# Kernel optimization log

Hardware: AMD Instinct MI355X
Metric: run time of the kernel (lower is better)

## Reference

```python
import jax, jax.numpy as jnp
import numpy as np

N = 50000   # nodes
E = 600000  # edges
D = 128     # node_features (EvolveGCNO in=out channels)
H = 128     # hidden_dim (final Linear out)


def setup_inputs() -> dict:
    key = jax.random.key(0)
    ks = jax.random.split(key, 9)
    stdv = 1.0 / np.sqrt(D)
    u = lambda k, shape: jax.random.uniform(k, shape, jnp.float32, -stdv, stdv)
    return {
        "x": jax.random.normal(ks[0], (N, D), jnp.float32),
        "edge_index": jax.random.randint(ks[1], (2, E), 0, N),
        "edge_weight": jax.random.uniform(ks[2], (E,), jnp.float32),
        "W0": u(ks[3], (D, D)),        # EvolveGCNO initial_weight (squeezed)
        "w_ih": u(ks[4], (3 * D, D)),  # GRU input weights (r|z|n)
        "w_hh": u(ks[5], (3 * D, D)),  # GRU hidden weights (r|z|n)
        "b_ih": u(ks[6], (3 * D,)),
        "b_hh": u(ks[7], (3 * D,)),
        "W_lin": u(ks[8], (H, D)),     # torch Linear weight [out, in]
        "b_lin": jnp.zeros((H,), jnp.float32),
    }


def _gru_step(x, h, w_ih, w_hh, b_ih, b_hh):
    # One torch.nn.GRU cell step; here x == h == W0 (weight evolution).
    gi = x @ w_ih.T + b_ih
    gh = h @ w_hh.T + b_hh
    i_r, i_z, i_n = jnp.split(gi, 3, axis=-1)
    h_r, h_z, h_n = jnp.split(gh, 3, axis=-1)
    r = jax.nn.sigmoid(i_r + h_r)
    z = jax.nn.sigmoid(i_z + h_z)
    n = jnp.tanh(i_n + r * h_n)
    return (1.0 - z) * n + z * h


def reference(x, edge_index, edge_weight, W0, w_ih, w_hh, b_ih, b_hh, W_lin, b_lin):
    # 1) Evolve the GCN weight with one GRU step (input = hidden = W0).
    W = _gru_step(W0, W0, w_ih, w_hh, b_ih, b_hh)  # [D, D]

    # 2) GCNConv_Fixed_W: add self-loops (weight 1), symmetric normalization.
    loops = jnp.arange(N)
    row = jnp.concatenate([edge_index[0], loops])  # source
    col = jnp.concatenate([edge_index[1], loops])  # target
    ew = jnp.concatenate([edge_weight, jnp.ones((N,), x.dtype)])
    deg = jax.ops.segment_sum(ew, col, num_segments=N)
    dinv = jnp.where(deg > 0, jax.lax.rsqrt(deg), 0.0)
    norm = dinv[row] * ew * dinv[col]  # [E+N]

    xw = x @ W                                        # [N, D]
    h = jax.ops.segment_sum(norm[:, None] * xw[row], col, num_segments=N)  # [N, D]

    # 3) ReLU + Linear
    h = jax.nn.relu(h)
    return h @ W_lin.T + b_lin  # [N, H]
```

## Files before the change

### kernel.cpp

```cpp
#include <hip/hip_runtime.h>
#include <hip/hip_bf16.h>

#define NN 50000
#define EE 600000
#define DD 128
#define CAP 48
#define CNT_SHIFT 25
#define SUM_MASK 0x1FFFFFFu

typedef __attribute__((ext_vector_type(8))) __bf16 bf16x8;
typedef __attribute__((ext_vector_type(8))) short short8;
typedef __attribute__((ext_vector_type(4))) float f32x4;

__device__ __forceinline__ unsigned short f2bf(float f) {
    union { float f; unsigned u; } c; c.f = f;
    unsigned r = (c.u + 0x7fffu + ((c.u >> 16) & 1u)) >> 16;
    return (unsigned short)r;
}
__device__ __forceinline__ float bflo(unsigned u) {
    union { unsigned u; float f; } c; c.u = u << 16; return c.f;
}
__device__ __forceinline__ float bfhi(unsigned u) {
    union { unsigned u; float f; } c; c.u = u & 0xffff0000u; return c.f;
}
__device__ __forceinline__ float degof(unsigned p) {
    return 1.0f + (float)(p & SUM_MASK) * (1.0f / 65536.0f);
}

__global__ __launch_bounds__(256) void init_gru_kernel(
    unsigned* __restrict__ cnt32,
    const float* __restrict__ W0, const float* __restrict__ w_ih,
    const float* __restrict__ w_hh, const float* __restrict__ b_ih,
    const float* __restrict__ b_hh, unsigned short* __restrict__ Wbt)
{
    if (blockIdx.x < 49) {
        int i = blockIdx.x * 256 + threadIdx.x;
        if (i < 50176 * 4 / 16) ((uint4*)cnt32)[i] = make_uint4(0u, 0u, 0u, 0u);
        return;
    }
    int idx = (blockIdx.x - 49) * 256 + threadIdx.x;
    int i = idx >> 7, j = idx & 127;
    const float4* a  = (const float4*)(W0  + i * DD);
    const float4* pr = (const float4*)(w_ih + (j        ) * DD);
    const float4* pz = (const float4*)(w_ih + (j + 128  ) * DD);
    const float4* pn = (const float4*)(w_ih + (j + 256  ) * DD);
    const float4* qr = (const float4*)(w_hh + (j        ) * DD);
    const float4* qz = (const float4*)(w_hh + (j + 128  ) * DD);
    const float4* qn = (const float4*)(w_hh + (j + 256  ) * DD);
    float ir = 0.f, iz = 0.f, inn = 0.f, hr = 0.f, hz = 0.f, hn = 0.f;
    for (int d = 0; d < DD / 4; ++d) {
        float4 av = a[d];
        float4 t;
        t = pr[d]; ir  += av.x*t.x + av.y*t.y + av.z*t.z + av.w*t.w;
        t = pz[d]; iz  += av.x*t.x + av.y*t.y + av.z*t.z + av.w*t.w;
        t = pn[d]; inn += av.x*t.x + av.y*t.y + av.z*t.z + av.w*t.w;
        t = qr[d]; hr  += av.x*t.x + av.y*t.y + av.z*t.z + av.w*t.w;
        t = qz[d]; hz  += av.x*t.x + av.y*t.y + av.z*t.z + av.w*t.w;
        t = qn[d]; hn  += av.x*t.x + av.y*t.y + av.z*t.z + av.w*t.w;
    }
    ir += b_ih[j]; iz += b_ih[j + 128]; inn += b_ih[j + 256];
    hr += b_hh[j]; hz += b_hh[j + 128]; hn  += b_hh[j + 256];
    float r = 1.f / (1.f + expf(-(ir + hr)));
    float z = 1.f / (1.f + expf(-(iz + hz)));
    float n = tanhf(inn + r * hn);
    float w = (1.f - z) * n + z * W0[idx];
    Wbt[j * DD + i] = f2bf(w);
}

__global__ __launch_bounds__(256) void histfill_kernel(
    const int* __restrict__ row, const int* __restrict__ col,
    const float* __restrict__ ew,
    unsigned* __restrict__ cnt32, unsigned* __restrict__ edges)
{
    int e = blockIdx.x * 256 + threadIdx.x;
    if (e >= EE) return;
    int c = col[e];
    unsigned wq = (unsigned)(ew[e] * 65536.0f);
    if (wq > 65535u) wq = 65535u;
    unsigned old = atomicAdd(&cnt32[c], (1u << CNT_SHIFT) | wq);
    unsigned oldcnt = old >> CNT_SHIFT;
    if (oldcnt < CAP)
        edges[(size_t)c * CAP + oldcnt] = (unsigned)row[e] | (wq << 16);
}

__global__ __launch_bounds__(256) void gather_kernel(
    const unsigned* __restrict__ edges, const unsigned* __restrict__ cnt32,
    const unsigned* __restrict__ xwu, unsigned* __restrict__ hu)
{
    int wid  = threadIdx.x >> 6;
    int lane = threadIdx.x & 63;
    int node = blockIdx.x * 4 + wid;
    if (node >= NN) return;
    unsigned pn = cnt32[node];
    int n = (int)(pn >> CNT_SHIFT); if (n > CAP) n = CAP;
    const unsigned* eb = edges + (size_t)node * CAP;
    float ax = 0.f, ay = 0.f;
    int k = 0;
    int n8 = n & ~7;
    for (; k < n8; k += 8) {
        uint4 ra = *(const uint4*)(eb + k);
        uint4 rb = *(const uint4*)(eb + k + 4);
        int s0 = (int)(ra.x & 0xFFFFu), s1 = (int)(ra.y & 0xFFFFu);
        int s2 = (int)(ra.z & 0xFFFFu), s3 = (int)(ra.w & 0xFFFFu);
        int s4 = (int)(rb.x & 0xFFFFu), s5 = (int)(rb.y & 0xFFFFu);
        int s6 = (int)(rb.z & 0xFFFFu), s7 = (int)(rb.w & 0xFFFFu);
        unsigned p0 = cnt32[s0], p1 = cnt32[s1], p2 = cnt32[s2], p3 = cnt32[s3];
        unsigned p4 = cnt32[s4], p5 = cnt32[s5], p6 = cnt32[s6], p7 = cnt32[s7];
        unsigned x0 = xwu[(size_t)s0 * 64 + lane];
        unsigned x1 = xwu[(size_t)s1 * 64 + lane];
        unsigned x2 = xwu[(size_t)s2 * 64 + lane];
        unsigned x3 = xwu[(size_t)s3 * 64 + lane];
        unsigned x4 = xwu[(size_t)s4 * 64 + lane];
        unsigned x5 = xwu[(size_t)s5 * 64 + lane];
        unsigned x6 = xwu[(size_t)s6 * 64 + lane];
        unsigned x7 = xwu[(size_t)s7 * 64 + lane];
        float v0 = (float)(ra.x >> 16) * (1.0f / 65536.0f) * rsqrtf(degof(p0));
        float v1 = (float)(ra.y >> 16) * (1.0f / 65536.0f) * rsqrtf(degof(p1));
        float v2 = (float)(ra.z >> 16) * (1.0f / 65536.0f) * rsqrtf(degof(p2));
        float v3 = (float)(ra.w >> 16) * (1.0f / 65536.0f) * rsqrtf(degof(p3));
        float v4 = (float)(rb.x >> 16) * (1.0f / 65536.0f) * rsqrtf(degof(p4));
        float v5 = (float)(rb.y >> 16) * (1.0f / 65536.0f) * rsqrtf(degof(p5));
        float v6 = (float)(rb.z >> 16) * (1.0f / 65536.0f) * rsqrtf(degof(p6));
        float v7 = (float)(rb.w >> 16) * (1.0f / 65536.0f) * rsqrtf(degof(p7));
        ax += v0 * bflo(x0) + v1 * bflo(x1) + v2 * bflo(x2) + v3 * bflo(x3)
            + v4 * bflo(x4) + v5 * bflo(x5) + v6 * bflo(x6) + v7 * bflo(x7);
        ay += v0 * bfhi(x0) + v1 * bfhi(x1) + v2 * bfhi(x2) + v3 * bfhi(x3)
            + v4 * bfhi(x4) + v5 * bfhi(x5) + v6 * bfhi(x6) + v7 * bfhi(x7);
    }
    int n4 = n & ~3;
    for (; k < n4; k += 4) {
        uint4 rc = *(const uint4*)(eb + k);
        int s0 = (int)(rc.x & 0xFFFFu), s1 = (int)(rc.y & 0xFFFFu);
        int s2 = (int)(rc.z & 0xFFFFu), s3 = (int)(rc.w & 0xFFFFu);
        unsigned p0 = cnt32[s0], p1 = cnt32[s1], p2 = cnt32[s2], p3 = cnt32[s3];
        unsigned x0 = xwu[(size_t)s0 * 64 + lane];
        unsigned x1 = xwu[(size_t)s1 * 64 + lane];
        unsigned x2 = xwu[(size_t)s2 * 64 + lane];
        unsigned x3 = xwu[(size_t)s3 * 64 + lane];
        float v0 = (float)(rc.x >> 16) * (1.0f / 65536.0f) * rsqrtf(degof(p0));
        float v1 = (float)(rc.y >> 16) * (1.0f / 65536.0f) * rsqrtf(degof(p1));
        float v2 = (float)(rc.z >> 16) * (1.0f / 65536.0f) * rsqrtf(degof(p2));
        float v3 = (float)(rc.w >> 16) * (1.0f / 65536.0f) * rsqrtf(degof(p3));
        ax += v0 * bflo(x0) + v1 * bflo(x1) + v2 * bflo(x2) + v3 * bflo(x3);
        ay += v0 * bfhi(x0) + v1 * bfhi(x1) + v2 * bfhi(x2) + v3 * bfhi(x3);
    }
    for (; k < n; ++k) {
        unsigned r0 = eb[k];
        int s0 = (int)(r0 & 0xFFFFu);
        unsigned p0 = cnt32[s0];
        unsigned x0 = xwu[(size_t)s0 * 64 + lane];
        float v0 = (float)(r0 >> 16) * (1.0f / 65536.0f) * rsqrtf(degof(p0));
        ax += v0 * bflo(x0); ay += v0 * bfhi(x0);
    }
    float s = rsqrtf(degof(pn));
    hu[(size_t)node * 64 + lane] =
        (unsigned)f2bf(ax * s) | ((unsigned)f2bf(ay * s) << 16);
}

template <int MODE>
__global__ __launch_bounds__(256) void mfma_gemm(
    const float* __restrict__ Af, const short* __restrict__ hb,
    const short* __restrict__ xwb, const unsigned* __restrict__ cnt32,
    const short* __restrict__ Bb, const float* __restrict__ Bf,
    const float* __restrict__ bias,
    unsigned short* __restrict__ outb, float* __restrict__ outf)
{
    __shared__ __align__(16) short Bs[DD * DD];
    __shared__ __align__(16) short As[64 * DD];
    const int t = threadIdx.x;
    const int i0 = blockIdx.x * 64;

    if (MODE == 0) {
        for (int u = t; u < 2048; u += 256) {
            int byte = u << 4;
            int brow = byte >> 8;
            *(short8*)((char*)Bs + (byte ^ ((brow & 7) << 4))) =
                *(const short8*)((const char*)Bb + byte);
        }
    } else {
        for (int u = t; u < 2048; u += 256) {
            int brow = u >> 4;
            int kc = (u & 15) << 3;
            const float4* p = (const float4*)(Bf + brow * DD + kc);
            float4 f0 = p[0], f1 = p[1];
            short8 v;
            v[0] = (short)f2bf(f0.x); v[1] = (short)f2bf(f0.y);
            v[2] = (short)f2bf(f0.z); v[3] = (short)f2bf(f0.w);
            v[4] = (short)f2bf(f1.x); v[5] = (short)f2bf(f1.y);
            v[6] = (short)f2bf(f1.z); v[7] = (short)f2bf(f1.w);
            int byte = (brow << 8) + (kc << 1);
            *(short8*)((char*)Bs + (byte ^ ((brow & 7) << 4))) = v;
        }
    }

    for (int u = t; u < 1024; u += 256) {
        int arow = u >> 4;
        int kc = (u & 15) << 3;
        int grow = i0 + arow;
        short8 v;
#pragma unroll
        for (int i = 0; i < 8; ++i) v[i] = 0;
        if (grow < NN) {
            if (MODE == 0) {
                const float4* p = (const float4*)(Af + (size_t)grow * DD + kc);
                float4 f0 = p[0], f1 = p[1];
                v[0] = (short)f2bf(f0.x); v[1] = (short)f2bf(f0.y);
                v[2] = (short)f2bf(f0.z); v[3] = (short)f2bf(f0.w);
                v[4] = (short)f2bf(f1.x); v[5] = (short)f2bf(f1.y);
                v[6] = (short)f2bf(f1.z); v[7] = (short)f2bf(f1.w);
            } else {
                float s = 1.0f / degof(cnt32[grow]);
                uint4 hu = *(const uint4*)(hb  + (size_t)grow * DD + kc);
                uint4 xu = *(const uint4*)(xwb + (size_t)grow * DD + kc);
                v[0] = (short)f2bf(fmaxf(bflo(hu.x) + s * bflo(xu.x), 0.f));
                v[1] = (short)f2bf(fmaxf(bfhi(hu.x) + s * bfhi(xu.x), 0.f));
                v[2] = (short)f2bf(fmaxf(bflo(hu.y) + s * bflo(xu.y), 0.f));
                v[3] = (short)f2bf(fmaxf(bfhi(hu.y) + s * bfhi(xu.y), 0.f));
                v[4] = (short)f2bf(fmaxf(bflo(hu.z) + s * bflo(xu.z), 0.f));
                v[5] = (short)f2bf(fmaxf(bfhi(hu.z) + s * bfhi(xu.z), 0.f));
                v[6] = (short)f2bf(fmaxf(bflo(hu.w) + s * bflo(xu.w), 0.f));
                v[7] = (short)f2bf(fmaxf(bfhi(hu.w) + s * bfhi(xu.w), 0.f));
            }
        }
        int byte = (arow << 8) + (kc << 1);
        *(short8*)((char*)As + (byte ^ ((arow & 7) << 4))) = v;
    }
    __syncthreads();

    const int lane = t & 63, wv = t >> 6;
    const int c0 = lane & 15, g = lane >> 4;
    const int arow = wv * 16 + c0;
    f32x4 acc[8];
#pragma unroll
    for (int n = 0; n < 8; ++n) { acc[n][0] = acc[n][1] = acc[n][2] = acc[n][3] = 0.f; }

#pragma unroll
    for (int s = 0; s < 4; ++s) {
        int k0 = s * 32 + g * 8;
        int abyte = (arow << 8) + (k0 << 1);
        bf16x8 a = *(const bf16x8*)((const char*)As + (abyte ^ ((arow & 7) << 4)));
#pragma unroll
        for (int n = 0; n < 8; ++n) {
            int bcol = n * 16 + c0;
            int bbyte = (bcol << 8) + (k0 << 1);
            bf16x8 b = *(const bf16x8*)((const char*)Bs + (bbyte ^ ((bcol & 7) << 4)));
            acc[n] = __builtin_amdgcn_mfma_f32_16x16x32_bf16(a, b, acc[n], 0, 0, 0);
        }
    }

#pragma unroll
    for (int n = 0; n < 8; ++n) {
        int ccol = n * 16 + c0;
        float bb = (MODE == 1) ? bias[ccol] : 0.f;
#pragma unroll
        for (int r = 0; r < 4; ++r) {
            int grow = i0 + wv * 16 + g * 4 + r;
            if (grow < NN) {
                if (MODE == 0)
                    outb[(size_t)grow * DD + ccol] = f2bf(acc[n][r]);
                else
                    outf[(size_t)grow * DD + ccol] = acc[n][r] + bb;
            }
        }
    }
}

extern "C" void kernel_launch(void* const* d_in, const int* in_sizes, int n_in,
                              void* d_out, int out_size, void* d_ws, size_t ws_size,
                              hipStream_t stream)
{
    const float* x    = (const float*)d_in[0];
    const int*   ei   = (const int*)d_in[1];
    const float* ew   = (const float*)d_in[2];
    const float* W0   = (const float*)d_in[3];
    const float* w_ih = (const float*)d_in[4];
    const float* w_hh = (const float*)d_in[5];
    const float* b_ih = (const float*)d_in[6];
    const float* b_hh = (const float*)d_in[7];
    const float* Wlin = (const float*)d_in[8];
    const float* blin = (const float*)d_in[9];
    float* out = (float*)d_out;

    const int* row = ei;
    const int* col = ei + EE;

    char* ws = (char*)d_ws;
    unsigned short* Wbt = (unsigned short*)ws;
    unsigned* cnt32 = (unsigned*)(ws + 32768);
    short* xw   = (short*)(ws + 233472);
    short* h    = (short*)(ws + 13033472);
    unsigned* edges = (unsigned*)(ws + 25833472);

    init_gru_kernel<<<113, 256, 0, stream>>>(cnt32, W0, w_ih, w_hh, b_ih, b_hh, Wbt);

    histfill_kernel<<<(EE + 255) / 256, 256, 0, stream>>>(row, col, ew, cnt32, edges);

    mfma_gemm<0><<<(NN + 63) / 64, 256, 0, stream>>>(
        x, nullptr, nullptr, nullptr, (const short*)Wbt, nullptr, nullptr,
        (unsigned short*)xw, nullptr);

    gather_kernel<<<(NN + 3) / 4, 256, 0, stream>>>(
        edges, cnt32, (const unsigned*)xw, (unsigned*)h);

    mfma_gemm<1><<<(NN + 63) / 64, 256, 0, stream>>>(
        nullptr, h, xw, cnt32, nullptr, Wlin, blin, nullptr, out);
}
```

Measured before the change: 131.0 us.

## Aggregate raw bf16 features first, then fuse both GEMMs into one kernel

Reorders the GCN computation to aggregate bf16-converted x over neighbors (A·X) before multiplying by the evolved weight, using associativity. The x→bf16 conversion is folded into the init kernel, and the self-loop term is added inside the gather. The two GEMMs (agg@W then relu then @W_lin + bias) run in one kernel, with the intermediate kept in shared memory. This removes one kernel launch and the xw write/read round trip, at the cost of doubled LDS use per block (lower occupancy) and a slightly different rounding order.

```diff
diff --git a/kernel.cpp b/kernel.cpp
--- a/kernel.cpp
+++ b/kernel.cpp
@@ -27,12 +27,27 @@
     return 1.0f + (float)(p & SUM_MASK) * (1.0f / 65536.0f);
 }
 
-__global__ __launch_bounds__(256) void init_gru_kernel(
+__global__ __launch_bounds__(256) void init_kernel(
     unsigned* __restrict__ cnt32,
     const float* __restrict__ W0, const float* __restrict__ w_ih,
     const float* __restrict__ w_hh, const float* __restrict__ b_ih,
-    const float* __restrict__ b_hh, unsigned short* __restrict__ Wbt)
-{
+    const float* __restrict__ b_hh, unsigned short* __restrict__ Wbt,
+    const float* __restrict__ x, short* __restrict__ xb)
+{
+    if (blockIdx.x >= 113) {
+        int u = (blockIdx.x - 113) * 256 + threadIdx.x;
+        if (u < NN * DD / 8) {
+            const float4* p = (const float4*)x + (size_t)u * 2;
+            float4 f0 = p[0], f1 = p[1];
+            short8 v;
+            v[0] = (short)f2bf(f0.x); v[1] = (short)f2bf(f0.y);
+            v[2] = (short)f2bf(f0.z); v[3] = (short)f2bf(f0.w);
+            v[4] = (short)f2bf(f1.x); v[5] = (short)f2bf(f1.y);
+            v[6] = (short)f2bf(f1.z); v[7] = (short)f2bf(f1.w);
+            *(short8*)(xb + (size_t)u * 8) = v;
+        }
+        return;
+    }
     if (blockIdx.x < 49) {
         int i = blockIdx.x * 256 + threadIdx.x;
         if (i < 50176 * 4 / 16) ((uint4*)cnt32)[i] = make_uint4(0u, 0u, 0u, 0u);
@@ -85,7 +100,7 @@
 
 __global__ __launch_bounds__(256) void gather_kernel(
     const unsigned* __restrict__ edges, const unsigned* __restrict__ cnt32,
-    const unsigned* __restrict__ xwu, unsigned* __restrict__ hu)
+    const unsigned* __restrict__ xbu, unsigned* __restrict__ aggu)
 {
     int wid  = threadIdx.x >> 6;
     int lane = threadIdx.x & 63;
@@ -94,7 +109,9 @@
     unsigned pn = cnt32[node];
     int n = (int)(pn >> CNT_SHIFT); if (n > CAP) n = CAP;
     const unsigned* eb = edges + (size_t)node * CAP;
-    float ax = 0.f, ay = 0.f;
+    float s = rsqrtf(degof(pn));
+    unsigned xs = xbu[(size_t)node * 64 + lane];
+    float ax = s * bflo(xs), ay = s * bfhi(xs);
     int k = 0;
     int n8 = n & ~7;
     for (; k < n8; k += 8) {
@@ -106,14 +123,14 @@
         int s6 = (int)(rb.z & 0xFFFFu), s7 = (int)(rb.w & 0xFFFFu);
         unsigned p0 = cnt32[s0], p1 = cnt32[s1], p2 = cnt32[s2], p3 = cnt32[s3];
         unsigned p4 = cnt32[s4], p5 = cnt32[s5], p6 = cnt32[s6], p7 = cnt32[s7];
-        unsigned x0 = xwu[(size_t)s0 * 64 + lane];
-        unsigned x1 = xwu[(size_t)s1 * 64 + lane];
-        unsigned x2 = xwu[(size_t)s2 * 64 + lane];
-        unsigned x3 = xwu[(size_t)s3 * 64 + lane];
-        unsigned x4 = xwu[(size_t)s4 * 64 + lane];
-        unsigned x5 = xwu[(size_t)s5 * 64 + lane];
-        unsigned x6 = xwu[(size_t)s6 * 64 + lane];
-        unsigned x7 = xwu[(size_t)s7 * 64 + lane];
+        unsigned x0 = xbu[(size_t)s0 * 64 + lane];
+        unsigned x1 = xbu[(size_t)s1 * 64 + lane];
+        unsigned x2 = xbu[(size_t)s2 * 64 + lane];
+        unsigned x3 = xbu[(size_t)s3 * 64 + lane];
+        unsigned x4 = xbu[(size_t)s4 * 64 + lane];
+        unsigned x5 = xbu[(size_t)s5 * 64 + lane];
+        unsigned x6 = xbu[(size_t)s6 * 64 + lane];
+        unsigned x7 = xbu[(size_t)s7 * 64 + lane];
         float v0 = (float)(ra.x >> 16) * (1.0f / 65536.0f) * rsqrtf(degof(p0));
         float v1 = (float)(ra.y >> 16) * (1.0f / 65536.0f) * rsqrtf(degof(p1));
         float v2 = (float)(ra.z >> 16) * (1.0f / 65536.0f) * rsqrtf(degof(p2));
@@ -133,10 +150,10 @@
         int s0 = (int)(rc.x & 0xFFFFu), s1 = (int)(rc.y & 0xFFFFu);
         int s2 = (int)(rc.z & 0xFFFFu), s3 = (int)(rc.w & 0xFFFFu);
         unsigned p0 = cnt32[s0], p1 = cnt32[s1], p2 = cnt32[s2], p3 = cnt32[s3];
-        unsigned x0 = xwu[(size_t)s0 * 64 + lane];
-        unsigned x1 = xwu[(size_t)s1 * 64 + lane];
-        unsigned x2 = xwu[(size_t)s2 * 64 + lane];
-        unsigned x3 = xwu[(size_t)s3 * 64 + lane];
+        unsigned x0 = xbu[(size_t)s0 * 64 + lane];
+        unsigned x1 = xbu[(size_t)s1 * 64 + lane];
+        unsigned x2 = xbu[(size_t)s2 * 64 + lane];
+        unsigned x3 = xbu[(size_t)s3 * 64 + lane];
         float v0 = (float)(rc.x >> 16) * (1.0f / 65536.0f) * rsqrtf(degof(p0));
         float v1 = (float)(rc.y >> 16) * (1.0f / 65536.0f) * rsqrtf(degof(p1));
         float v2 = (float)(rc.z >> 16) * (1.0f / 65536.0f) * rsqrtf(degof(p2));
@@ -148,51 +165,44 @@
         unsigned r0 = eb[k];
         int s0 = (int)(r0 & 0xFFFFu);
         unsigned p0 = cnt32[s0];
-        unsigned x0 = xwu[(size_t)s0 * 64 + lane];
+        unsigned x0 = xbu[(size_t)s0 * 64 + lane];
         float v0 = (float)(r0 >> 16) * (1.0f / 65536.0f) * rsqrtf(degof(p0));
         ax += v0 * bflo(x0); ay += v0 * bfhi(x0);
     }
-    float s = rsqrtf(degof(pn));
-    hu[(size_t)node * 64 + lane] =
+    aggu[(size_t)node * 64 + lane] =
         (unsigned)f2bf(ax * s) | ((unsigned)f2bf(ay * s) << 16);
 }
 
-template <int MODE>
-__global__ __launch_bounds__(256) void mfma_gemm(
-    const float* __restrict__ Af, const short* __restrict__ hb,
-    const short* __restrict__ xwb, const unsigned* __restrict__ cnt32,
-    const short* __restrict__ Bb, const float* __restrict__ Bf,
-    const float* __restrict__ bias,
-    unsigned short* __restrict__ outb, float* __restrict__ outf)
-{
-    __shared__ __align__(16) short Bs[DD * DD];
+__global__ __launch_bounds__(256) void fused_gemm(
+    const short* __restrict__ agg, const short* __restrict__ Wbt,
+    const float* __restrict__ Wlin, const float* __restrict__ bias,
+    float* __restrict__ out)
+{
+    __shared__ __align__(16) short Bs1[DD * DD];
+    __shared__ __align__(16) short Bs2[DD * DD];
     __shared__ __align__(16) short As[64 * DD];
     const int t = threadIdx.x;
     const int i0 = blockIdx.x * 64;
 
-    if (MODE == 0) {
-        for (int u = t; u < 2048; u += 256) {
-            int byte = u << 4;
-            int brow = byte >> 8;
-            *(short8*)((char*)Bs + (byte ^ ((brow & 7) << 4))) =
-                *(const short8*)((const char*)Bb + byte);
-        }
-    } else {
-        for (int u = t; u < 2048; u += 256) {
-            int brow = u >> 4;
-            int kc = (u & 15) << 3;
-            const float4* p = (const float4*)(Bf + brow * DD + kc);
-            float4 f0 = p[0], f1 = p[1];
-            short8 v;
-            v[0] = (short)f2bf(f0.x); v[1] = (short)f2bf(f0.y);
-            v[2] = (short)f2bf(f0.z); v[3] = (short)f2bf(f0.w);
-            v[4] = (short)f2bf(f1.x); v[5] = (short)f2bf(f1.y);
-            v[6] = (short)f2bf(f1.z); v[7] = (short)f2bf(f1.w);
-            int byte = (brow << 8) + (kc << 1);
-            *(short8*)((char*)Bs + (byte ^ ((brow & 7) << 4))) = v;
-        }
-    }
-
+    for (int u = t; u < 2048; u += 256) {
+        int byte = u << 4;
+        int brow = byte >> 8;
+        *(short8*)((char*)Bs1 + (byte ^ ((brow & 7) << 4))) =
+            *(const short8*)((const char*)Wbt + byte);
+    }
+    for (int u = t; u < 2048; u += 256) {
+        int brow = u >> 4;
+        int kc = (u & 15) << 3;
+        const float4* p = (const float4*)(Wlin + brow * DD + kc);
+        float4 f0 = p[0], f1 = p[1];
+        short8 v;
+        v[0] = (short)f2bf(f0.x); v[1] = (short)f2bf(f0.y);
+        v[2] = (short)f2bf(f0.z); v[3] = (short)f2bf(f0.w);
+        v[4] = (short)f2bf(f1.x); v[5] = (short)f2bf(f1.y);
+        v[6] = (short)f2bf(f1.z); v[7] = (short)f2bf(f1.w);
+        int byte = (brow << 8) + (kc << 1);
+        *(short8*)((char*)Bs2 + (byte ^ ((brow & 7) << 4))) = v;
+    }
     for (int u = t; u < 1024; u += 256) {
         int arow = u >> 4;
         int kc = (u & 15) << 3;
@@ -200,28 +210,8 @@
         short8 v;
 #pragma unroll
         for (int i = 0; i < 8; ++i) v[i] = 0;
-        if (grow < NN) {
-            if (MODE == 0) {
-                const float4* p = (const float4*)(Af + (size_t)grow * DD + kc);
-                float4 f0 = p[0], f1 = p[1];
-                v[0] = (short)f2bf(f0.x); v[1] = (short)f2bf(f0.y);
-                v[2] = (short)f2bf(f0.z); v[3] = (short)f2bf(f0.w);
-                v[4] = (short)f2bf(f1.x); v[5] = (short)f2bf(f1.y);
-                v[6] = (short)f2bf(f1.z); v[7] = (short)f2bf(f1.w);
-            } else {
-                float s = 1.0f / degof(cnt32[grow]);
-                uint4 hu = *(const uint4*)(hb  + (size_t)grow * DD + kc);
-                uint4 xu = *(const uint4*)(xwb + (size_t)grow * DD + kc);
-                v[0] = (short)f2bf(fmaxf(bflo(hu.x) + s * bflo(xu.x), 0.f));
-                v[1] = (short)f2bf(fmaxf(bfhi(hu.x) + s * bfhi(xu.x), 0.f));
-                v[2] = (short)f2bf(fmaxf(bflo(hu.y) + s * bflo(xu.y), 0.f));
-                v[3] = (short)f2bf(fmaxf(bfhi(hu.y) + s * bfhi(xu.y), 0.f));
-                v[4] = (short)f2bf(fmaxf(bflo(hu.z) + s * bflo(xu.z), 0.f));
-                v[5] = (short)f2bf(fmaxf(bfhi(hu.z) + s * bfhi(xu.z), 0.f));
-                v[6] = (short)f2bf(fmaxf(bflo(hu.w) + s * bflo(xu.w), 0.f));
-                v[7] = (short)f2bf(fmaxf(bfhi(hu.w) + s * bfhi(xu.w), 0.f));
-            }
-        }
+        if (grow < NN)
+            v = *(const short8*)(agg + (size_t)grow * DD + kc);
         int byte = (arow << 8) + (kc << 1);
         *(short8*)((char*)As + (byte ^ ((arow & 7) << 4))) = v;
     }
@@ -243,24 +233,51 @@
         for (int n = 0; n < 8; ++n) {
             int bcol = n * 16 + c0;
             int bbyte = (bcol << 8) + (k0 << 1);
-            bf16x8 b = *(const bf16x8*)((const char*)Bs + (bbyte ^ ((bcol & 7) << 4)));
+            bf16x8 b = *(const bf16x8*)((const char*)Bs1 + (bbyte ^ ((bcol & 7) << 4)));
             acc[n] = __builtin_amdgcn_mfma_f32_16x16x32_bf16(a, b, acc[n], 0, 0, 0);
         }
     }
+    __syncthreads();
 
 #pragma unroll
     for (int n = 0; n < 8; ++n) {
         int ccol = n * 16 + c0;
-        float bb = (MODE == 1) ? bias[ccol] : 0.f;
+#pragma unroll
+        for (int r = 0; r < 4; ++r) {
+            int hrow = wv * 16 + g * 4 + r;
+            int byte = (hrow << 8) + (ccol << 1);
+            *(unsigned short*)((char*)As + (byte ^ ((hrow & 7) << 4))) =
+                f2bf(fmaxf(acc[n][r], 0.f));
+        }
+    }
+    __syncthreads();
+
+#pragma unroll
+    for (int n = 0; n < 8; ++n) { acc[n][0] = acc[n][1] = acc[n][2] = acc[n][3] = 0.f; }
+
+#pragma unroll
+    for (int s = 0; s < 4; ++s) {
+        int k0 = s * 32 + g * 8;
+        int abyte = (arow << 8) + (k0 << 1);
+        bf16x8 a = *(const bf16x8*)((const char*)As + (abyte ^ ((arow & 7) << 4)));
+#pragma unroll
+        for (int n = 0; n < 8; ++n) {
+            int bcol = n * 16 + c0;
+            int bbyte = (bcol << 8) + (k0 << 1);
+            bf16x8 b = *(const bf16x8*)((const char*)Bs2 + (bbyte ^ ((bcol & 7) << 4)));
+            acc[n] = __builtin_amdgcn_mfma_f32_16x16x32_bf16(a, b, acc[n], 0, 0, 0);
+        }
+    }
+
+#pragma unroll
+    for (int n = 0; n < 8; ++n) {
+        int ccol = n * 16 + c0;
+        float bb = bias[ccol];
 #pragma unroll
         for (int r = 0; r < 4; ++r) {
             int grow = i0 + wv * 16 + g * 4 + r;
-            if (grow < NN) {
-                if (MODE == 0)
-                    outb[(size_t)grow * DD + ccol] = f2bf(acc[n][r]);
-                else
-                    outf[(size_t)grow * DD + ccol] = acc[n][r] + bb;
-            }
+            if (grow < NN)
+                out[(size_t)grow * DD + ccol] = acc[n][r] + bb;
         }
     }
 }
@@ -287,21 +304,17 @@
     char* ws = (char*)d_ws;
     unsigned short* Wbt = (unsigned short*)ws;
     unsigned* cnt32 = (unsigned*)(ws + 32768);
-    short* xw   = (short*)(ws + 233472);
-    short* h    = (short*)(ws + 13033472);
+    short* xb   = (short*)(ws + 233472);
+    short* agg  = (short*)(ws + 13033472);
     unsigned* edges = (unsigned*)(ws + 25833472);
 
-    init_gru_kernel<<<113, 256, 0, stream>>>(cnt32, W0, w_ih, w_hh, b_ih, b_hh, Wbt);
+    init_kernel<<<3238, 256, 0, stream>>>(cnt32, W0, w_ih, w_hh, b_ih, b_hh, Wbt, x, xb);
 
     histfill_kernel<<<(EE + 255) / 256, 256, 0, stream>>>(row, col, ew, cnt32, edges);
 
-    mfma_gemm<0><<<(NN + 63) / 64, 256, 0, stream>>>(
-        x, nullptr, nullptr, nullptr, (const short*)Wbt, nullptr, nullptr,
-        (unsigned short*)xw, nullptr);
-
     gather_kernel<<<(NN + 3) / 4, 256, 0, stream>>>(
-        edges, cnt32, (const unsigned*)xw, (unsigned*)h);
-
-    mfma_gemm<1><<<(NN + 63) / 64, 256, 0, stream>>>(
-        nullptr, h, xw, cnt32, nullptr, Wlin, blin, nullptr, out);
-}
+        edges, cnt32, (const unsigned*)xb, (unsigned*)agg);
+
+    fused_gemm<<<(NN + 63) / 64, 256, 0, stream>>>(
+        agg, (const short*)Wbt, Wlin, blin, out);
+}
```

New measurement: 121.2 us. 1.08x faster.
